# Optimization experiments

Measured on AMD Instinct MI355X. Metric: run time of the kernel, lower is better.

## Reference

```python
import jax, jax.numpy as jnp
import numpy as np

N, E, D, H = 100000, 1250000, 64, 128
EPS = 1e-5


def sage_bn_relu(x, src, dst, W_self, b_self, W_neigh, gamma, beta):
    # mean aggregation over in-neighbors (DGL SAGEConv 'mean')
    n = x.shape[0]
    deg = jax.ops.segment_sum(jnp.ones((src.shape[0],), x.dtype), dst, num_segments=n)
    agg = jax.ops.segment_sum(x[src], dst, num_segments=n)  # [N, d]
    neigh = agg / jnp.maximum(deg, 1.0)[:, None]             # zero in-degree -> 0
    h = x @ W_self + b_self + neigh @ W_neigh                # fc_self + fc_neigh
    # BatchNorm1d (training-mode batch statistics, biased variance)
    mu = h.mean(0)
    var = jnp.mean((h - mu) ** 2, axis=0)
    h = (h - mu) * jax.lax.rsqrt(var + EPS) * gamma + beta
    return jax.nn.relu(h)  # dropout omitted (deterministic eval)


def setup_inputs() -> dict:
    key = jax.random.key(0)
    ks = jax.random.split(key, 32)
    inp = {
        "x": jax.random.normal(ks[0], (N, D), jnp.float32),
        "src": jax.random.randint(ks[1], (E,), 0, N),
        "dst": jax.random.randint(ks[2], (E,), 0, N),
    }
    dims = [(D, H), (H, H), (H, H)]
    k = 3
    for i, (din, dout) in enumerate(dims):
        s = 1.0 / np.sqrt(din)
        inp[f"W_self{i}"] = jax.random.uniform(ks[k], (din, dout), jnp.float32, -s, s); k += 1
        inp[f"b_self{i}"] = jnp.zeros((dout,), jnp.float32)
        inp[f"W_neigh{i}"] = jax.random.uniform(ks[k], (din, dout), jnp.float32, -s, s); k += 1
        inp[f"gamma{i}"] = jnp.ones((dout,), jnp.float32)
        inp[f"beta{i}"] = jnp.zeros((dout,), jnp.float32)
    s = 1.0 / np.sqrt(H)
    inp["Wc"] = jax.random.uniform(ks[k], (H, 2), jnp.float32, -s, s)
    inp["bc"] = jnp.zeros((2,), jnp.float32)
    return inp


def reference(x, src, dst,
              W_self0, b_self0, W_neigh0, gamma0, beta0,
              W_self1, b_self1, W_neigh1, gamma1, beta1,
              W_self2, b_self2, W_neigh2, gamma2, beta2,
              Wc, bc):
    h = sage_bn_relu(x, src, dst, W_self0, b_self0, W_neigh0, gamma0, beta0)
    h = sage_bn_relu(h, src, dst, W_self1, b_self1, W_neigh1, gamma1, beta1)
    h = sage_bn_relu(h, src, dst, W_self2, b_self2, W_neigh2, gamma2, beta2)
    return h @ Wc + bc  # [N, 2]
```

## Files before the change

### kernel.cpp

```cpp
#include <hip/hip_runtime.h>


#define N_NODES 100000
#define N_EDGES 1250000
#define NB 1042
#define BSZ 96
#define CAP 1536
#define BPART 256
#define INVN (1.0f / 100000.0f)

typedef short bf16x8 __attribute__((ext_vector_type(8)));
typedef float f32x4 __attribute__((ext_vector_type(4)));
typedef unsigned short u16x8 __attribute__((ext_vector_type(8)));
typedef unsigned short u16x4 __attribute__((ext_vector_type(4)));

__device__ __forceinline__ float bf2f(unsigned short u) {
  union { unsigned int i; float f; } c; c.i = ((unsigned int)u) << 16; return c.f;
}
__device__ __forceinline__ unsigned short f2bf(float f) {
  union { float f; unsigned int i; } c; c.f = f;
  unsigned int r = (c.i + 0x7FFFu + ((c.i >> 16) & 1u)) >> 16;
  return (unsigned short)r;
}
__device__ __forceinline__ void bn_st(const float* stats, const float* gam,
                                      const float* bet, int c, float& s, float& t) {
  float sum = stats[c] + stats[256 + c] + stats[512 + c] + stats[768 + c];
  float sq  = stats[128 + c] + stats[384 + c] + stats[640 + c] + stats[896 + c];
  float mu = sum * INVN;
  float var = sq * INVN - mu * mu;
  s = gam[c] * rsqrtf(var + 1e-5f);
  t = bet[c] - mu * s;
}
__device__ __forceinline__ void gload_lds16(const void* g, void* l) {
  __builtin_amdgcn_global_load_lds(
      (const __attribute__((address_space(1))) unsigned int*)g,
      (__attribute__((address_space(3))) unsigned int*)l, 16, 0, 0);
}

__global__ __launch_bounds__(256) void k_prep(
    const float* __restrict__ x, unsigned short* __restrict__ x16,
    const float* __restrict__ W0s, const float* __restrict__ W0n,
    const float* __restrict__ W1s, const float* __restrict__ W1n,
    const float* __restrict__ W2s, const float* __restrict__ W2n,
    unsigned short* __restrict__ wt, int* __restrict__ gcursor,
    float* __restrict__ stats3) {
  int blk = blockIdx.x, t = threadIdx.x;
  if (blk < 6250) {
    int i = blk * 256 + t;
    float4 v = ((const float4*)x)[i];
    u16x4 o;
    o.x = f2bf(v.x); o.y = f2bf(v.y); o.z = f2bf(v.z); o.w = f2bf(v.w);
    ((u16x4*)x16)[i] = o;
  } else if (blk < 6570) {
    int i = (blk - 6250) * 256 + t;
    if (i < 16384) {
      const float* W = (i < 8192) ? W0s : W0n;
      unsigned short* o = wt + (i < 8192 ? 0 : 8192);
      int j = i & 8191;
      int c = j >> 6, k = j & 63;
      o[j] = f2bf(W[k * 128 + c]);
    } else {
      int j = i - 16384;
      int sel = j >> 14;
      j &= 16383;
      const float* W = (sel == 0) ? W1s : (sel == 1) ? W1n : (sel == 2) ? W2s : W2n;
      unsigned short* o = wt + 16384 + sel * 16384;
      int c = j >> 7, k = j & 127;
      o[j] = f2bf(W[k * 128 + c]);
    }
  } else {
    for (int i = t; i < NB; i += 256) gcursor[i] = 0;
    for (int i = t; i < 3 * 1024; i += 256) stats3[i] = 0.f;
  }
}

__global__ __launch_bounds__(256) void k_hist(const int* __restrict__ dst,
                                              int* __restrict__ hist, int E) {
  __shared__ int h[NB];
  int t = threadIdx.x;
  int chunk = (E + BPART - 1) / BPART;
  int start = blockIdx.x * chunk;
  int end = min(E, start + chunk);
  for (int b = t; b < NB; b += 256) h[b] = 0;
  __syncthreads();
  for (int e = start + t; e < end; e += 256) atomicAdd(&h[dst[e] / BSZ], 1);
  __syncthreads();
  for (int b = t; b < NB; b += 256) hist[blockIdx.x * NB + b] = h[b];
}

__global__ __launch_bounds__(256) void k_scan(const int* __restrict__ hist,
                                              int* __restrict__ base,
                                              int* __restrict__ gcursor) {
  int bb = blockIdx.x * 256 + threadIdx.x;
  if (bb >= NB) return;
  int run = 0;
  for (int r0 = 0; r0 < BPART; r0 += 16) {
    int v[16];
    #pragma unroll
    for (int u = 0; u < 16; u++) v[u] = hist[(r0 + u) * NB + bb];
    #pragma unroll
    for (int u = 0; u < 16; u++) { base[(r0 + u) * NB + bb] = run; run += v[u]; }
  }
  gcursor[bb] = run;
}

__global__ __launch_bounds__(256) void k_scatter(const int* __restrict__ src,
                                                 const int* __restrict__ dst,
                                                 const int* __restrict__ base,
                                                 unsigned int* __restrict__ part, int E) {
  __shared__ int cur[NB];
  int t = threadIdx.x;
  int chunk = (E + BPART - 1) / BPART;
  int start = blockIdx.x * chunk;
  int end = min(E, start + chunk);
  for (int b = t; b < NB; b += 256) cur[b] = base[blockIdx.x * NB + b];
  __syncthreads();
  for (int e = start + t; e < end; e += 256) {
    int d = dst[e];
    int b = d / BSZ;
    int pos = atomicAdd(&cur[b], 1);
    if ((unsigned)pos < (unsigned)CAP)
      part[(size_t)b * CAP + pos] = (unsigned)src[e] | ((unsigned)(d - b * BSZ) << 17);
  }
}

template <int DIM>
__global__ __launch_bounds__(512) void k_aggb(const unsigned short* __restrict__ h,
                                              const unsigned int* __restrict__ part,
                                              const int* __restrict__ gcursor,
                                              unsigned short* __restrict__ neigh, int n,
                                              const float* __restrict__ statsP,
                                              const float* __restrict__ gamP,
                                              const float* __restrict__ betP) {
  __shared__ unsigned eraw[CAP];
  __shared__ unsigned eord[CAP];
  __shared__ int cnt[BSZ], offv[BSZ], cur[BSZ];
  __shared__ int scan[128];
  int t = threadIdx.x;
  int bkt = blockIdx.x;
  int node0 = bkt * BSZ;
  int nn = min(BSZ, n - node0);
  if (nn <= 0) return;
  if (t < BSZ) cnt[t] = 0;
  __syncthreads();
  int ec = gcursor[bkt];
  ec = max(0, min(ec, CAP));
  for (int i = t; i < ec; i += 512) {
    unsigned w = part[(size_t)bkt * CAP + i];
    eraw[i] = w;
    atomicAdd(&cnt[w >> 17], 1);
  }
  __syncthreads();
  if (t < 128) scan[t] = (t < BSZ) ? cnt[t] : 0;
  __syncthreads();
  #pragma unroll
  for (int o = 1; o < 128; o <<= 1) {
    int x = 0;
    if (t < 128 && t >= o) x = scan[t - o];
    __syncthreads();
    if (t < 128) scan[t] += x;
    __syncthreads();
  }
  if (t < BSZ) { offv[t] = scan[t] - cnt[t]; cur[t] = scan[t] - cnt[t]; }
  __syncthreads();
  for (int i = t; i < ec; i += 512) {
    unsigned w = eraw[i];
    int p = atomicAdd(&cur[w >> 17], 1);
    eord[p] = w & 0x1FFFF;
  }
  __syncthreads();
  const int G = DIM / 8, NG = 512 / G;
  int gid = t / G, li = t % G;
  float sreg[8], treg[8];
  bool bn = (statsP != nullptr);
  if (bn) {
    #pragma unroll
    for (int k = 0; k < 8; k++) bn_st(statsP, gamP, betP, li * 8 + k, sreg[k], treg[k]);
  }
  for (int nd = gid; nd < nn; nd += NG) {
    int s = offv[nd], c = cnt[nd];
    int e = s + c;
    float acc[8] = {0.f, 0.f, 0.f, 0.f, 0.f, 0.f, 0.f, 0.f};
    int j = s;
    for (; j + 4 <= e; j += 4) {
      int sn0 = eord[j], sn1 = eord[j + 1], sn2 = eord[j + 2], sn3 = eord[j + 3];
      u16x8 v0 = *(const u16x8*)&h[(size_t)sn0 * DIM + li * 8];
      u16x8 v1 = *(const u16x8*)&h[(size_t)sn1 * DIM + li * 8];
      u16x8 v2 = *(const u16x8*)&h[(size_t)sn2 * DIM + li * 8];
      u16x8 v3 = *(const u16x8*)&h[(size_t)sn3 * DIM + li * 8];
      if (bn) {
        #pragma unroll
        for (int k = 0; k < 8; k++)
          acc[k] += fmaxf(fmaf(bf2f(v0[k]), sreg[k], treg[k]), 0.f)
                  + fmaxf(fmaf(bf2f(v1[k]), sreg[k], treg[k]), 0.f)
                  + fmaxf(fmaf(bf2f(v2[k]), sreg[k], treg[k]), 0.f)
                  + fmaxf(fmaf(bf2f(v3[k]), sreg[k], treg[k]), 0.f);
      } else {
        #pragma unroll
        for (int k = 0; k < 8; k++)
          acc[k] += (bf2f(v0[k]) + bf2f(v1[k])) + (bf2f(v2[k]) + bf2f(v3[k]));
      }
    }
    for (; j + 2 <= e; j += 2) {
      int sn0 = eord[j], sn1 = eord[j + 1];
      u16x8 v0 = *(const u16x8*)&h[(size_t)sn0 * DIM + li * 8];
      u16x8 v1 = *(const u16x8*)&h[(size_t)sn1 * DIM + li * 8];
      if (bn) {
        #pragma unroll
        for (int k = 0; k < 8; k++)
          acc[k] += fmaxf(fmaf(bf2f(v0[k]), sreg[k], treg[k]), 0.f)
                  + fmaxf(fmaf(bf2f(v1[k]), sreg[k], treg[k]), 0.f);
      } else {
        #pragma unroll
        for (int k = 0; k < 8; k++) acc[k] += bf2f(v0[k]) + bf2f(v1[k]);
      }
    }
    if (j < e) {
      int sn = eord[j];
      u16x8 v = *(const u16x8*)&h[(size_t)sn * DIM + li * 8];
      if (bn) {
        #pragma unroll
        for (int k = 0; k < 8; k++)
          acc[k] += fmaxf(fmaf(bf2f(v[k]), sreg[k], treg[k]), 0.f);
      } else {
        #pragma unroll
        for (int k = 0; k < 8; k++) acc[k] += bf2f(v[k]);
      }
    }
    float inv = 1.0f / fmaxf((float)c, 1.0f);
    u16x8 o;
    #pragma unroll
    for (int k = 0; k < 8; k++) o[k] = f2bf(acc[k] * inv);
    *(u16x8*)&neigh[(size_t)(node0 + nd) * DIM + li * 8] = o;
  }
}

__global__ __launch_bounds__(256) void k_gemm_mfma(
    const unsigned short* __restrict__ A1, const unsigned short* __restrict__ W1t,
    const unsigned short* __restrict__ A2, const unsigned short* __restrict__ W2t,
    const float* __restrict__ bias, unsigned short* __restrict__ C,
    float* __restrict__ stats, int M, int din,
    const float* __restrict__ statsP, const float* __restrict__ gamP,
    const float* __restrict__ betP) {
  __shared__ unsigned short As[2][128 * 32];
  __shared__ unsigned short Bs[2][128 * 32];
  __shared__ float redS[4 * 128];
  __shared__ float redQ[4 * 128];
  __shared__ float sBN[128], tBN[128];

  int t = threadIdx.x;
  int lane = t & 63, w = t >> 6;
  int l15 = lane & 15, quad = lane >> 4;
  int row0 = blockIdx.x * 128;
  bool hasBN = (statsP != nullptr);
  if (hasBN && t < 128) bn_st(statsP, gamP, betP, t, sBN[t], tBN[t]);
  if (hasBN) __syncthreads();

  const int steps1 = din >> 5;
  const int S = steps1 * 2;

  f32x4 acc[2][8];
  #pragma unroll
  for (int rt = 0; rt < 2; rt++)
    #pragma unroll
    for (int ct = 0; ct < 8; ct++) acc[rt][ct] = (f32x4){0.f, 0.f, 0.f, 0.f};

  auto Aof  = [&](int s) { return (s < steps1) ? A1 : A2; };
  auto Wof  = [&](int s) { return (s < steps1) ? W1t : W2t; };
  auto k0of = [&](int s) { return ((s < steps1) ? s : s - steps1) << 5; };

  auto stageA_async = [&](int s, int bi) {
    const unsigned short* A = Aof(s); int k0 = k0of(s);
    #pragma unroll
    for (int i = 0; i < 2; i++) {
      int idx = t + 256 * i;
      int r = idx >> 2, prt = idx & 3;
      gload_lds16(&A[(size_t)(row0 + r) * din + k0 + prt * 8],
                  &As[bi][(i * 256 + w * 64) * 8]);
    }
  };
  auto stageB = [&](int s, int bi) {
    const unsigned short* Wt = Wof(s); int k0 = k0of(s);
    #pragma unroll
    for (int i = 0; i < 2; i++) {
      int idx = t + 256 * i;
      int r = idx >> 2, prt = idx & 3;
      gload_lds16(&Wt[(size_t)r * din + k0 + prt * 8],
                  &Bs[bi][(i * 256 + w * 64) * 8]);
    }
  };
  u16x8 vreg[2];
  auto bnLoad = [&](int s) {
    const unsigned short* A = Aof(s); int k0 = k0of(s);
    #pragma unroll
    for (int i = 0; i < 2; i++) {
      int idx = t + 256 * i;
      int r = idx >> 2, prt = idx & 3;
      int row = row0 + r;
      vreg[i] = (u16x8){0, 0, 0, 0, 0, 0, 0, 0};
      if (row < M) vreg[i] = *(const u16x8*)&A[(size_t)row * din + k0 + prt * 8];
    }
  };
  auto bnWrite = [&](int s, int bi) {
    int k0 = k0of(s);
    #pragma unroll
    for (int i = 0; i < 2; i++) {
      int idx = t + 256 * i;
      int prt = idx & 3;
      u16x8 v = vreg[i];
      #pragma unroll
      for (int j = 0; j < 8; j++) {
        int c = k0 + prt * 8 + j;
        v[j] = f2bf(fmaxf(fmaf(bf2f(v[j]), sBN[c], tBN[c]), 0.f));
      }
      *(u16x8*)&As[bi][idx * 8] = v;
    }
  };

  if (hasBN) { bnLoad(0); stageB(0, 0); bnWrite(0, 0); }
  else       { stageA_async(0, 0); stageB(0, 0); }
  __syncthreads();

  int cb = 0;
  for (int s = 0; s < S; s++) {
    int nb = cb ^ 1;
    bool haveNext = (s + 1 < S);
    bool bnNext = hasBN && (s + 1 < steps1);
    if (haveNext) {
      if (bnNext) bnLoad(s + 1);
      else        stageA_async(s + 1, nb);
      stageB(s + 1, nb);
    }
    bf16x8 af[2], bfr[8];
    #pragma unroll
    for (int rt = 0; rt < 2; rt++)
      af[rt] = *(const bf16x8*)&As[cb][(w * 32 + rt * 16 + l15) * 32 + quad * 8];
    #pragma unroll
    for (int ct = 0; ct < 8; ct++)
      bfr[ct] = *(const bf16x8*)&Bs[cb][(ct * 16 + l15) * 32 + quad * 8];
    #pragma unroll
    for (int rt = 0; rt < 2; rt++)
      #pragma unroll
      for (int ct = 0; ct < 8; ct++)
        acc[rt][ct] = __builtin_amdgcn_mfma_f32_16x16x32_bf16(af[rt], bfr[ct], acc[rt][ct], 0, 0, 0);
    if (haveNext) {
      if (bnNext) bnWrite(s + 1, nb);
      __syncthreads();
    }
    cb = nb;
  }

  float bcol[8], ls[8], lq[8];
  #pragma unroll
  for (int ct = 0; ct < 8; ct++) {
    bcol[ct] = bias[ct * 16 + l15];
    ls[ct] = 0.f; lq[ct] = 0.f;
  }
  #pragma unroll
  for (int rt = 0; rt < 2; rt++) {
    #pragma unroll
    for (int r = 0; r < 4; r++) {
      int row = row0 + w * 32 + rt * 16 + quad * 4 + r;
      if (row < M) {
        #pragma unroll
        for (int ct = 0; ct < 8; ct++) {
          float v = acc[rt][ct][r] + bcol[ct];
          C[(size_t)row * 128 + ct * 16 + l15] = f2bf(v);
          ls[ct] += v; lq[ct] += v * v;
        }
      }
    }
  }
  #pragma unroll
  for (int ct = 0; ct < 8; ct++) {
    ls[ct] += __shfl_xor(ls[ct], 16); ls[ct] += __shfl_xor(ls[ct], 32);
    lq[ct] += __shfl_xor(lq[ct], 16); lq[ct] += __shfl_xor(lq[ct], 32);
  }
  if (quad == 0) {
    #pragma unroll
    for (int ct = 0; ct < 8; ct++) {
      redS[w * 128 + ct * 16 + l15] = ls[ct];
      redQ[w * 128 + ct * 16 + l15] = lq[ct];
    }
  }
  __syncthreads();
  if (t < 128) {
    float s = redS[t] + redS[128 + t] + redS[256 + t] + redS[384 + t];
    float q = redQ[t] + redQ[128 + t] + redQ[256 + t] + redQ[384 + t];
    int rep = (blockIdx.x & 3) * 256;
    atomicAdd(&stats[rep + t], s);
    atomicAdd(&stats[rep + 128 + t], q);
  }
}

__global__ void k_final(const unsigned short* __restrict__ h,
                        const float* __restrict__ statsP, const float* __restrict__ gamP,
                        const float* __restrict__ betP, const float* __restrict__ Wc,
                        const float* __restrict__ bc, float* __restrict__ out, int n) {
  int lane = threadIdx.x & 63;
  int row = blockIdx.x * (blockDim.x >> 6) + (threadIdx.x >> 6);
  if (row >= n) return;
  float acc0 = 0.f, acc1 = 0.f;
  #pragma unroll
  for (int m = 0; m < 2; m++) {
    int c = lane + 64 * m;
    float s, tt;
    bn_st(statsP, gamP, betP, c, s, tt);
    float v = bf2f(h[(size_t)row * 128 + c]);
    v = fmaxf(fmaf(v, s, tt), 0.f);
    acc0 += v * Wc[c * 2 + 0];
    acc1 += v * Wc[c * 2 + 1];
  }
  #pragma unroll
  for (int off = 32; off > 0; off >>= 1) {
    acc0 += __shfl_down(acc0, off);
    acc1 += __shfl_down(acc1, off);
  }
  if (lane == 0) {
    out[row * 2 + 0] = acc0 + bc[0];
    out[row * 2 + 1] = acc1 + bc[1];
  }
}

extern "C" void kernel_launch(void* const* d_in, const int* in_sizes, int n_in,
                              void* d_out, int out_size, void* d_ws, size_t ws_size,
                              hipStream_t stream) {
  const float* x   = (const float*)d_in[0];
  const int* src   = (const int*)d_in[1];
  const int* dst   = (const int*)d_in[2];
  const float* Wself[3] = {(const float*)d_in[3], (const float*)d_in[8],  (const float*)d_in[13]};
  const float* bself[3] = {(const float*)d_in[4], (const float*)d_in[9],  (const float*)d_in[14]};
  const float* Wngh[3]  = {(const float*)d_in[5], (const float*)d_in[10], (const float*)d_in[15]};
  const float* gam[3]   = {(const float*)d_in[6], (const float*)d_in[11], (const float*)d_in[16]};
  const float* bet[3]   = {(const float*)d_in[7], (const float*)d_in[12], (const float*)d_in[17]};
  const float* Wc = (const float*)d_in[18];
  const float* bc = (const float*)d_in[19];
  float* out = (float*)d_out;

  const int N = N_NODES, E = N_EDGES;

  unsigned short* x16 = (unsigned short*)d_ws;
  unsigned short* b0  = x16 + (size_t)N * 64;
  unsigned short* b1  = b0 + (size_t)N * 128;
  unsigned short* b2  = b1 + (size_t)N * 128;
  unsigned short* wt  = b2 + (size_t)N * 128;
  unsigned int* part  = (unsigned int*)(wt + 81920);
  int* gcursor  = (int*)(part + (size_t)NB * CAP);
  float* stats3 = (float*)(gcursor + NB);

  int* hist = (int*)b1;
  int* base = hist + (size_t)BPART * NB;

  k_prep<<<6571, 256, 0, stream>>>(x, x16, Wself[0], Wngh[0], Wself[1], Wngh[1],
                                   Wself[2], Wngh[2], wt, gcursor, stats3);

  k_hist<<<BPART, 256, 0, stream>>>(dst, hist, E);
  k_scan<<<(NB + 255) / 256, 256, 0, stream>>>(hist, base, gcursor);
  k_scatter<<<BPART, 256, 0, stream>>>(src, dst, base, part, E);

  const int gemmBlocks = (N + 127) / 128;

  k_aggb<64><<<NB, 512, 0, stream>>>(x16, part, gcursor, b0, N, nullptr, nullptr, nullptr);
  k_gemm_mfma<<<gemmBlocks, 256, 0, stream>>>(x16, wt + 0, b0, wt + 8192, bself[0],
                                              b1, stats3 + 0, N, 64,
                                              nullptr, nullptr, nullptr);

  k_aggb<128><<<NB, 512, 0, stream>>>(b1, part, gcursor, b0, N,
                                      stats3 + 0, gam[0], bet[0]);
  k_gemm_mfma<<<gemmBlocks, 256, 0, stream>>>(b1, wt + 16384, b0, wt + 32768, bself[1],
                                              b2, stats3 + 1024, N, 128,
                                              stats3 + 0, gam[0], bet[0]);

  k_aggb<128><<<NB, 512, 0, stream>>>(b2, part, gcursor, b0, N,
                                      stats3 + 1024, gam[1], bet[1]);
  k_gemm_mfma<<<gemmBlocks, 256, 0, stream>>>(b2, wt + 49152, b0, wt + 65536, bself[2],
                                              b1, stats3 + 2048, N, 128,
                                              stats3 + 1024, gam[1], bet[1]);

  k_final<<<(N + 3) / 4, 256, 0, stream>>>(b1, stats3 + 2048, gam[2], bet[2],
                                           Wc, bc, out, N);
}
```

Measured before the change: 398.9 us.

## Unfuse BatchNorm+ReLU into a standalone in-place pass before aggregation

```diff
diff --git a/kernel.cpp b/kernel.cpp
--- a/kernel.cpp
+++ b/kernel.cpp
@@ -42,8 +42,7 @@
     const float* __restrict__ W0s, const float* __restrict__ W0n,
     const float* __restrict__ W1s, const float* __restrict__ W1n,
     const float* __restrict__ W2s, const float* __restrict__ W2n,
-    unsigned short* __restrict__ wt, int* __restrict__ gcursor,
-    float* __restrict__ stats3) {
+    unsigned short* __restrict__ wt, float* __restrict__ stats3) {
   int blk = blockIdx.x, t = threadIdx.x;
   if (blk < 6250) {
     int i = blk * 256 + t;
@@ -69,7 +68,6 @@
       o[j] = f2bf(W[k * 128 + c]);
     }
   } else {
-    for (int i = t; i < NB; i += 256) gcursor[i] = 0;
     for (int i = t; i < 3 * 1024; i += 256) stats3[i] = 0.f;
   }
 }
@@ -124,14 +122,29 @@
   }
 }
 
+__global__ __launch_bounds__(256) void k_bnrelu(unsigned short* __restrict__ h,
+                                                const float* __restrict__ statsP,
+                                                const float* __restrict__ gamP,
+                                                const float* __restrict__ betP, int n8) {
+  __shared__ float sS[128], sT[128];
+  int t = threadIdx.x;
+  if (t < 128) bn_st(statsP, gamP, betP, t, sS[t], sT[t]);
+  __syncthreads();
+  int i = blockIdx.x * 256 + t;
+  if (i >= n8) return;
+  int c0 = (i & 15) * 8;
+  u16x8 v = ((const u16x8*)h)[i];
+  #pragma unroll
+  for (int j = 0; j < 8; j++)
+    v[j] = f2bf(fmaxf(fmaf(bf2f(v[j]), sS[c0 + j], sT[c0 + j]), 0.f));
+  ((u16x8*)h)[i] = v;
+}
+
 template <int DIM>
 __global__ __launch_bounds__(512) void k_aggb(const unsigned short* __restrict__ h,
                                               const unsigned int* __restrict__ part,
                                               const int* __restrict__ gcursor,
-                                              unsigned short* __restrict__ neigh, int n,
-                                              const float* __restrict__ statsP,
-                                              const float* __restrict__ gamP,
-                                              const float* __restrict__ betP) {
+                                              unsigned short* __restrict__ neigh, int n) {
   __shared__ unsigned eraw[CAP];
   __shared__ unsigned eord[CAP];
   __shared__ int cnt[BSZ], offv[BSZ], cur[BSZ];
@@ -171,61 +184,23 @@
   __syncthreads();
   const int G = DIM / 8, NG = 512 / G;
   int gid = t / G, li = t % G;
-  float sreg[8], treg[8];
-  bool bn = (statsP != nullptr);
-  if (bn) {
-    #pragma unroll
-    for (int k = 0; k < 8; k++) bn_st(statsP, gamP, betP, li * 8 + k, sreg[k], treg[k]);
-  }
   for (int nd = gid; nd < nn; nd += NG) {
     int s = offv[nd], c = cnt[nd];
     int e = s + c;
     float acc[8] = {0.f, 0.f, 0.f, 0.f, 0.f, 0.f, 0.f, 0.f};
     int j = s;
-    for (; j + 4 <= e; j += 4) {
-      int sn0 = eord[j], sn1 = eord[j + 1], sn2 = eord[j + 2], sn3 = eord[j + 3];
-      u16x8 v0 = *(const u16x8*)&h[(size_t)sn0 * DIM + li * 8];
-      u16x8 v1 = *(const u16x8*)&h[(size_t)sn1 * DIM + li * 8];
-      u16x8 v2 = *(const u16x8*)&h[(size_t)sn2 * DIM + li * 8];
-      u16x8 v3 = *(const u16x8*)&h[(size_t)sn3 * DIM + li * 8];
-      if (bn) {
-        #pragma unroll
-        for (int k = 0; k < 8; k++)
-          acc[k] += fmaxf(fmaf(bf2f(v0[k]), sreg[k], treg[k]), 0.f)
-                  + fmaxf(fmaf(bf2f(v1[k]), sreg[k], treg[k]), 0.f)
-                  + fmaxf(fmaf(bf2f(v2[k]), sreg[k], treg[k]), 0.f)
-                  + fmaxf(fmaf(bf2f(v3[k]), sreg[k], treg[k]), 0.f);
-      } else {
-        #pragma unroll
-        for (int k = 0; k < 8; k++)
-          acc[k] += (bf2f(v0[k]) + bf2f(v1[k])) + (bf2f(v2[k]) + bf2f(v3[k]));
-      }
-    }
     for (; j + 2 <= e; j += 2) {
       int sn0 = eord[j], sn1 = eord[j + 1];
       u16x8 v0 = *(const u16x8*)&h[(size_t)sn0 * DIM + li * 8];
       u16x8 v1 = *(const u16x8*)&h[(size_t)sn1 * DIM + li * 8];
-      if (bn) {
-        #pragma unroll
-        for (int k = 0; k < 8; k++)
-          acc[k] += fmaxf(fmaf(bf2f(v0[k]), sreg[k], treg[k]), 0.f)
-                  + fmaxf(fmaf(bf2f(v1[k]), sreg[k], treg[k]), 0.f);
-      } else {
-        #pragma unroll
-        for (int k = 0; k < 8; k++) acc[k] += bf2f(v0[k]) + bf2f(v1[k]);
-      }
+      #pragma unroll
+      for (int k = 0; k < 8; k++) acc[k] += bf2f(v0[k]) + bf2f(v1[k]);
     }
     if (j < e) {
       int sn = eord[j];
       u16x8 v = *(const u16x8*)&h[(size_t)sn * DIM + li * 8];
-      if (bn) {
-        #pragma unroll
-        for (int k = 0; k < 8; k++)
-          acc[k] += fmaxf(fmaf(bf2f(v[k]), sreg[k], treg[k]), 0.f);
-      } else {
-        #pragma unroll
-        for (int k = 0; k < 8; k++) acc[k] += bf2f(v[k]);
-      }
+      #pragma unroll
+      for (int k = 0; k < 8; k++) acc[k] += bf2f(v[k]);
     }
     float inv = 1.0f / fmaxf((float)c, 1.0f);
     u16x8 o;
@@ -239,22 +214,16 @@
     const unsigned short* __restrict__ A1, const unsigned short* __restrict__ W1t,
     const unsigned short* __restrict__ A2, const unsigned short* __restrict__ W2t,
     const float* __restrict__ bias, unsigned short* __restrict__ C,
-    float* __restrict__ stats, int M, int din,
-    const float* __restrict__ statsP, const float* __restrict__ gamP,
-    const float* __restrict__ betP) {
+    float* __restrict__ stats, int M, int din) {
   __shared__ unsigned short As[2][128 * 32];
   __shared__ unsigned short Bs[2][128 * 32];
   __shared__ float redS[4 * 128];
   __shared__ float redQ[4 * 128];
-  __shared__ float sBN[128], tBN[128];
 
   int t = threadIdx.x;
   int lane = t & 63, w = t >> 6;
   int l15 = lane & 15, quad = lane >> 4;
   int row0 = blockIdx.x * 128;
-  bool hasBN = (statsP != nullptr);
-  if (hasBN && t < 128) bn_st(statsP, gamP, betP, t, sBN[t], tBN[t]);
-  if (hasBN) __syncthreads();
 
   const int steps1 = din >> 5;
   const int S = steps1 * 2;
@@ -269,7 +238,7 @@
   auto Wof  = [&](int s) { return (s < steps1) ? W1t : W2t; };
   auto k0of = [&](int s) { return ((s < steps1) ? s : s - steps1) << 5; };
 
-  auto stageA_async = [&](int s, int bi) {
+  auto stageA = [&](int s, int bi) {
     const unsigned short* A = Aof(s); int k0 = k0of(s);
     #pragma unroll
     for (int i = 0; i < 2; i++) {
@@ -289,48 +258,15 @@
                   &Bs[bi][(i * 256 + w * 64) * 8]);
     }
   };
-  u16x8 vreg[2];
-  auto bnLoad = [&](int s) {
-    const unsigned short* A = Aof(s); int k0 = k0of(s);
-    #pragma unroll
-    for (int i = 0; i < 2; i++) {
-      int idx = t + 256 * i;
-      int r = idx >> 2, prt = idx & 3;
-      int row = row0 + r;
-      vreg[i] = (u16x8){0, 0, 0, 0, 0, 0, 0, 0};
-      if (row < M) vreg[i] = *(const u16x8*)&A[(size_t)row * din + k0 + prt * 8];
-    }
-  };
-  auto bnWrite = [&](int s, int bi) {
-    int k0 = k0of(s);
-    #pragma unroll
-    for (int i = 0; i < 2; i++) {
-      int idx = t + 256 * i;
-      int prt = idx & 3;
-      u16x8 v = vreg[i];
-      #pragma unroll
-      for (int j = 0; j < 8; j++) {
-        int c = k0 + prt * 8 + j;
-        v[j] = f2bf(fmaxf(fmaf(bf2f(v[j]), sBN[c], tBN[c]), 0.f));
-      }
-      *(u16x8*)&As[bi][idx * 8] = v;
-    }
-  };
-
-  if (hasBN) { bnLoad(0); stageB(0, 0); bnWrite(0, 0); }
-  else       { stageA_async(0, 0); stageB(0, 0); }
+
+  stageA(0, 0); stageB(0, 0);
   __syncthreads();
 
   int cb = 0;
   for (int s = 0; s < S; s++) {
     int nb = cb ^ 1;
     bool haveNext = (s + 1 < S);
-    bool bnNext = hasBN && (s + 1 < steps1);
-    if (haveNext) {
-      if (bnNext) bnLoad(s + 1);
-      else        stageA_async(s + 1, nb);
-      stageB(s + 1, nb);
-    }
+    if (haveNext) { stageA(s + 1, nb); stageB(s + 1, nb); }
     bf16x8 af[2], bfr[8];
     #pragma unroll
     for (int rt = 0; rt < 2; rt++)
@@ -343,10 +279,7 @@
       #pragma unroll
       for (int ct = 0; ct < 8; ct++)
         acc[rt][ct] = __builtin_amdgcn_mfma_f32_16x16x32_bf16(af[rt], bfr[ct], acc[rt][ct], 0, 0, 0);
-    if (haveNext) {
-      if (bnNext) bnWrite(s + 1, nb);
-      __syncthreads();
-    }
+    if (haveNext) __syncthreads();
     cb = nb;
   }
 
@@ -452,30 +385,28 @@
   int* base = hist + (size_t)BPART * NB;
 
   k_prep<<<6571, 256, 0, stream>>>(x, x16, Wself[0], Wngh[0], Wself[1], Wngh[1],
-                                   Wself[2], Wngh[2], wt, gcursor, stats3);
+                                   Wself[2], Wngh[2], wt, stats3);
 
   k_hist<<<BPART, 256, 0, stream>>>(dst, hist, E);
   k_scan<<<(NB + 255) / 256, 256, 0, stream>>>(hist, base, gcursor);
   k_scatter<<<BPART, 256, 0, stream>>>(src, dst, base, part, E);
 
   const int gemmBlocks = (N + 127) / 128;
-
-  k_aggb<64><<<NB, 512, 0, stream>>>(x16, part, gcursor, b0, N, nullptr, nullptr, nullptr);
+  const int bnBlocks = (N * 16 + 255) / 256;
+
+  k_aggb<64><<<NB, 512, 0, stream>>>(x16, part, gcursor, b0, N);
   k_gemm_mfma<<<gemmBlocks, 256, 0, stream>>>(x16, wt + 0, b0, wt + 8192, bself[0],
-                                              b1, stats3 + 0, N, 64,
-                                              nullptr, nullptr, nullptr);
-
-  k_aggb<128><<<NB, 512, 0, stream>>>(b1, part, gcursor, b0, N,
-                                      stats3 + 0, gam[0], bet[0]);
+                                              b1, stats3 + 0, N, 64);
+  k_bnrelu<<<bnBlocks, 256, 0, stream>>>(b1, stats3 + 0, gam[0], bet[0], N * 16);
+
+  k_aggb<128><<<NB, 512, 0, stream>>>(b1, part, gcursor, b0, N);
   k_gemm_mfma<<<gemmBlocks, 256, 0, stream>>>(b1, wt + 16384, b0, wt + 32768, bself[1],
-                                              b2, stats3 + 1024, N, 128,
-                                              stats3 + 0, gam[0], bet[0]);
-
-  k_aggb<128><<<NB, 512, 0, stream>>>(b2, part, gcursor, b0, N,
-                                      stats3 + 1024, gam[1], bet[1]);
+                                              b2, stats3 + 1024, N, 128);
+  k_bnrelu<<<bnBlocks, 256, 0, stream>>>(b2, stats3 + 1024, gam[1], bet[1], N * 16);
+
+  k_aggb<128><<<NB, 512, 0, stream>>>(b2, part, gcursor, b0, N);
   k_gemm_mfma<<<gemmBlocks, 256, 0, stream>>>(b2, wt + 49152, b0, wt + 65536, bself[2],
-                                              b1, stats3 + 2048, N, 128,
-                                              stats3 + 1024, gam[1], bet[1]);
+                                              b1, stats3 + 2048, N, 128);
 
   k_final<<<(N + 3) / 4, 256, 0, stream>>>(b1, stats3 + 2048, gam[2], bet[2],
                                            Wc, bc, out, N);
```

After: 416.5 us. 4.4% more time.

## Fuse neighbor aggregation into per-layer MFMA GEMM kernel via LDS tile

Applied to the files above, without the earlier changes.

```diff
diff --git a/kernel.cpp b/kernel.cpp
--- a/kernel.cpp
+++ b/kernel.cpp
@@ -3,9 +3,9 @@
 
 #define N_NODES 100000
 #define N_EDGES 1250000
-#define NB 1042
-#define BSZ 96
-#define CAP 1536
+#define NB 782
+#define BSZ 128
+#define CAP 2048
 #define BPART 256
 #define INVN (1.0f / 100000.0f)
 
@@ -36,14 +36,19 @@
       (const __attribute__((address_space(1))) unsigned int*)g,
       (__attribute__((address_space(3))) unsigned int*)l, 16, 0, 0);
 }
+template <int DIN>
+__device__ __forceinline__ int nswz(int row, int c) {
+  return row * DIN + (c ^ ((row & (DIN == 128 ? 15 : 7)) << 3));
+}
 
 __global__ __launch_bounds__(256) void k_prep(
     const float* __restrict__ x, unsigned short* __restrict__ x16,
     const float* __restrict__ W0s, const float* __restrict__ W0n,
     const float* __restrict__ W1s, const float* __restrict__ W1n,
     const float* __restrict__ W2s, const float* __restrict__ W2n,
-    unsigned short* __restrict__ wt, int* __restrict__ gcursor,
-    float* __restrict__ stats3) {
+    unsigned short* __restrict__ wt, float* __restrict__ stats3,
+    const int* __restrict__ dst, int* __restrict__ hist, int E) {
+  __shared__ int hh[NB];
   int blk = blockIdx.x, t = threadIdx.x;
   if (blk < 6250) {
     int i = blk * 256 + t;
@@ -68,24 +73,19 @@
       int c = j >> 7, k = j & 127;
       o[j] = f2bf(W[k * 128 + c]);
     }
+  } else if (blk == 6570) {
+    for (int i = t; i < 3 * 1024; i += 256) stats3[i] = 0.f;
   } else {
-    for (int i = t; i < NB; i += 256) gcursor[i] = 0;
-    for (int i = t; i < 3 * 1024; i += 256) stats3[i] = 0.f;
-  }
-}
-
-__global__ __launch_bounds__(256) void k_hist(const int* __restrict__ dst,
-                                              int* __restrict__ hist, int E) {
-  __shared__ int h[NB];
-  int t = threadIdx.x;
-  int chunk = (E + BPART - 1) / BPART;
-  int start = blockIdx.x * chunk;
-  int end = min(E, start + chunk);
-  for (int b = t; b < NB; b += 256) h[b] = 0;
-  __syncthreads();
-  for (int e = start + t; e < end; e += 256) atomicAdd(&h[dst[e] / BSZ], 1);
-  __syncthreads();
-  for (int b = t; b < NB; b += 256) hist[blockIdx.x * NB + b] = h[b];
+    int hb = blk - 6571;
+    int chunk = (E + BPART - 1) / BPART;
+    int start = hb * chunk;
+    int end = min(E, start + chunk);
+    for (int b = t; b < NB; b += 256) hh[b] = 0;
+    __syncthreads();
+    for (int e = start + t; e < end; e += 256) atomicAdd(&hh[dst[e] >> 7], 1);
+    __syncthreads();
+    for (int b = t; b < NB; b += 256) hist[hb * NB + b] = hh[b];
+  }
 }
 
 __global__ __launch_bounds__(256) void k_scan(const int* __restrict__ hist,
@@ -117,224 +117,205 @@
   __syncthreads();
   for (int e = start + t; e < end; e += 256) {
     int d = dst[e];
-    int b = d / BSZ;
+    int b = d >> 7;
     int pos = atomicAdd(&cur[b], 1);
     if ((unsigned)pos < (unsigned)CAP)
-      part[(size_t)b * CAP + pos] = (unsigned)src[e] | ((unsigned)(d - b * BSZ) << 17);
-  }
-}
-
-template <int DIM>
-__global__ __launch_bounds__(512) void k_aggb(const unsigned short* __restrict__ h,
-                                              const unsigned int* __restrict__ part,
-                                              const int* __restrict__ gcursor,
-                                              unsigned short* __restrict__ neigh, int n,
-                                              const float* __restrict__ statsP,
-                                              const float* __restrict__ gamP,
-                                              const float* __restrict__ betP) {
-  __shared__ unsigned eraw[CAP];
-  __shared__ unsigned eord[CAP];
-  __shared__ int cnt[BSZ], offv[BSZ], cur[BSZ];
-  __shared__ int scan[128];
-  int t = threadIdx.x;
-  int bkt = blockIdx.x;
-  int node0 = bkt * BSZ;
-  int nn = min(BSZ, n - node0);
-  if (nn <= 0) return;
-  if (t < BSZ) cnt[t] = 0;
-  __syncthreads();
-  int ec = gcursor[bkt];
-  ec = max(0, min(ec, CAP));
-  for (int i = t; i < ec; i += 512) {
-    unsigned w = part[(size_t)bkt * CAP + i];
-    eraw[i] = w;
-    atomicAdd(&cnt[w >> 17], 1);
-  }
-  __syncthreads();
-  if (t < 128) scan[t] = (t < BSZ) ? cnt[t] : 0;
-  __syncthreads();
-  #pragma unroll
-  for (int o = 1; o < 128; o <<= 1) {
-    int x = 0;
-    if (t < 128 && t >= o) x = scan[t - o];
-    __syncthreads();
-    if (t < 128) scan[t] += x;
-    __syncthreads();
-  }
-  if (t < BSZ) { offv[t] = scan[t] - cnt[t]; cur[t] = scan[t] - cnt[t]; }
-  __syncthreads();
-  for (int i = t; i < ec; i += 512) {
-    unsigned w = eraw[i];
-    int p = atomicAdd(&cur[w >> 17], 1);
-    eord[p] = w & 0x1FFFF;
-  }
-  __syncthreads();
-  const int G = DIM / 8, NG = 512 / G;
-  int gid = t / G, li = t % G;
-  float sreg[8], treg[8];
-  bool bn = (statsP != nullptr);
-  if (bn) {
-    #pragma unroll
-    for (int k = 0; k < 8; k++) bn_st(statsP, gamP, betP, li * 8 + k, sreg[k], treg[k]);
-  }
-  for (int nd = gid; nd < nn; nd += NG) {
-    int s = offv[nd], c = cnt[nd];
-    int e = s + c;
-    float acc[8] = {0.f, 0.f, 0.f, 0.f, 0.f, 0.f, 0.f, 0.f};
-    int j = s;
-    for (; j + 4 <= e; j += 4) {
-      int sn0 = eord[j], sn1 = eord[j + 1], sn2 = eord[j + 2], sn3 = eord[j + 3];
-      u16x8 v0 = *(const u16x8*)&h[(size_t)sn0 * DIM + li * 8];
-      u16x8 v1 = *(const u16x8*)&h[(size_t)sn1 * DIM + li * 8];
-      u16x8 v2 = *(const u16x8*)&h[(size_t)sn2 * DIM + li * 8];
-      u16x8 v3 = *(const u16x8*)&h[(size_t)sn3 * DIM + li * 8];
-      if (bn) {
-        #pragma unroll
-        for (int k = 0; k < 8; k++)
-          acc[k] += fmaxf(fmaf(bf2f(v0[k]), sreg[k], treg[k]), 0.f)
-                  + fmaxf(fmaf(bf2f(v1[k]), sreg[k], treg[k]), 0.f)
-                  + fmaxf(fmaf(bf2f(v2[k]), sreg[k], treg[k]), 0.f)
-                  + fmaxf(fmaf(bf2f(v3[k]), sreg[k], treg[k]), 0.f);
-      } else {
-        #pragma unroll
-        for (int k = 0; k < 8; k++)
-          acc[k] += (bf2f(v0[k]) + bf2f(v1[k])) + (bf2f(v2[k]) + bf2f(v3[k]));
-      }
-    }
-    for (; j + 2 <= e; j += 2) {
-      int sn0 = eord[j], sn1 = eord[j + 1];
-      u16x8 v0 = *(const u16x8*)&h[(size_t)sn0 * DIM + li * 8];
-      u16x8 v1 = *(const u16x8*)&h[(size_t)sn1 * DIM + li * 8];
-      if (bn) {
-        #pragma unroll
-        for (int k = 0; k < 8; k++)
-          acc[k] += fmaxf(fmaf(bf2f(v0[k]), sreg[k], treg[k]), 0.f)
-                  + fmaxf(fmaf(bf2f(v1[k]), sreg[k], treg[k]), 0.f);
-      } else {
-        #pragma unroll
-        for (int k = 0; k < 8; k++) acc[k] += bf2f(v0[k]) + bf2f(v1[k]);
-      }
-    }
-    if (j < e) {
-      int sn = eord[j];
-      u16x8 v = *(const u16x8*)&h[(size_t)sn * DIM + li * 8];
-      if (bn) {
-        #pragma unroll
-        for (int k = 0; k < 8; k++)
-          acc[k] += fmaxf(fmaf(bf2f(v[k]), sreg[k], treg[k]), 0.f);
-      } else {
-        #pragma unroll
-        for (int k = 0; k < 8; k++) acc[k] += bf2f(v[k]);
-      }
-    }
-    float inv = 1.0f / fmaxf((float)c, 1.0f);
-    u16x8 o;
-    #pragma unroll
-    for (int k = 0; k < 8; k++) o[k] = f2bf(acc[k] * inv);
-    *(u16x8*)&neigh[(size_t)(node0 + nd) * DIM + li * 8] = o;
-  }
-}
-
-__global__ __launch_bounds__(256) void k_gemm_mfma(
-    const unsigned short* __restrict__ A1, const unsigned short* __restrict__ W1t,
-    const unsigned short* __restrict__ A2, const unsigned short* __restrict__ W2t,
-    const float* __restrict__ bias, unsigned short* __restrict__ C,
-    float* __restrict__ stats, int M, int din,
+      part[(size_t)b * CAP + pos] = (unsigned)src[e] | ((unsigned)(d & 127) << 17);
+  }
+}
+
+template <int DIN, bool BN>
+__global__ __launch_bounds__(256) void k_layer(
+    const unsigned short* __restrict__ h, const unsigned short* __restrict__ W1t,
+    const unsigned short* __restrict__ W2t, const float* __restrict__ bias,
+    const unsigned int* __restrict__ part, const int* __restrict__ gcursor,
+    unsigned short* __restrict__ C, float* __restrict__ stats, int M,
     const float* __restrict__ statsP, const float* __restrict__ gamP,
     const float* __restrict__ betP) {
   __shared__ unsigned short As[2][128 * 32];
   __shared__ unsigned short Bs[2][128 * 32];
-  __shared__ float redS[4 * 128];
-  __shared__ float redQ[4 * 128];
+  __shared__ unsigned short neighT[128 * DIN];
+  __shared__ unsigned eord[CAP];
+  __shared__ int cnt[BSZ], offv[BSZ], cur[BSZ];
   __shared__ float sBN[128], tBN[128];
+  unsigned* eraw = (unsigned*)&As[0][0];
+  float* redS = (float*)&eord[0];
+  float* redQ = redS + 512;
 
   int t = threadIdx.x;
   int lane = t & 63, w = t >> 6;
   int l15 = lane & 15, quad = lane >> 4;
-  int row0 = blockIdx.x * 128;
-  bool hasBN = (statsP != nullptr);
-  if (hasBN && t < 128) bn_st(statsP, gamP, betP, t, sBN[t], tBN[t]);
-  if (hasBN) __syncthreads();
-
-  const int steps1 = din >> 5;
+  int bkt = blockIdx.x;
+  int node0 = bkt * BSZ;
+  int row0 = node0;
+  int nn = min(BSZ, M - node0);
+
+  if (t < BSZ) cnt[t] = 0;
+  if (BN && t < 128) bn_st(statsP, gamP, betP, t, sBN[t], tBN[t]);
+  __syncthreads();
+  int ec = gcursor[bkt];
+  ec = max(0, min(ec, CAP));
+  for (int i = t; i < ec; i += 256) {
+    unsigned wd = part[(size_t)bkt * CAP + i];
+    eraw[i] = wd;
+    atomicAdd(&cnt[wd >> 17], 1);
+  }
+  __syncthreads();
+  if (t < BSZ) offv[t] = cnt[t];
+  __syncthreads();
+  #pragma unroll
+  for (int o = 1; o < BSZ; o <<= 1) {
+    int xv = 0;
+    if (t < BSZ && t >= o) xv = offv[t - o];
+    __syncthreads();
+    if (t < BSZ) offv[t] += xv;
+    __syncthreads();
+  }
+  if (t < BSZ) { int ex = offv[t] - cnt[t]; offv[t] = ex; cur[t] = ex; }
+  __syncthreads();
+  for (int i = t; i < ec; i += 256) {
+    unsigned wd = eraw[i];
+    int p = atomicAdd(&cur[wd >> 17], 1);
+    eord[p] = wd & 0x1FFFF;
+  }
+  __syncthreads();
+
+  const int G = DIN / 8, NG = 256 / G;
+  int gid = t / G, li = t % G;
+  float sreg[8], treg[8];
+  if (BN) {
+    #pragma unroll
+    for (int k = 0; k < 8; k++) { sreg[k] = sBN[li * 8 + k]; treg[k] = tBN[li * 8 + k]; }
+  }
+  for (int nd = gid; nd < BSZ; nd += NG) {
+    u16x8 o;
+    if (nd >= nn) {
+      #pragma unroll
+      for (int k = 0; k < 8; k++) o[k] = 0;
+    } else {
+      int s0 = offv[nd], c = cnt[nd];
+      int e = s0 + c;
+      float acc[8] = {0.f, 0.f, 0.f, 0.f, 0.f, 0.f, 0.f, 0.f};
+      int j = s0;
+      for (; j + 4 <= e; j += 4) {
+        int a0 = eord[j], a1 = eord[j + 1], a2 = eord[j + 2], a3 = eord[j + 3];
+        u16x8 v0 = *(const u16x8*)&h[(size_t)a0 * DIN + li * 8];
+        u16x8 v1 = *(const u16x8*)&h[(size_t)a1 * DIN + li * 8];
+        u16x8 v2 = *(const u16x8*)&h[(size_t)a2 * DIN + li * 8];
+        u16x8 v3 = *(const u16x8*)&h[(size_t)a3 * DIN + li * 8];
+        if (BN) {
+          #pragma unroll
+          for (int k = 0; k < 8; k++)
+            acc[k] += fmaxf(fmaf(bf2f(v0[k]), sreg[k], treg[k]), 0.f)
+                    + fmaxf(fmaf(bf2f(v1[k]), sreg[k], treg[k]), 0.f)
+                    + fmaxf(fmaf(bf2f(v2[k]), sreg[k], treg[k]), 0.f)
+                    + fmaxf(fmaf(bf2f(v3[k]), sreg[k], treg[k]), 0.f);
+        } else {
+          #pragma unroll
+          for (int k = 0; k < 8; k++)
+            acc[k] += (bf2f(v0[k]) + bf2f(v1[k])) + (bf2f(v2[k]) + bf2f(v3[k]));
+        }
+      }
+      for (; j < e; j++) {
+        int a0 = eord[j];
+        u16x8 v0 = *(const u16x8*)&h[(size_t)a0 * DIN + li * 8];
+        #pragma unroll
+        for (int k = 0; k < 8; k++) {
+          float f = bf2f(v0[k]);
+          acc[k] += BN ? fmaxf(fmaf(f, sreg[k], treg[k]), 0.f) : f;
+        }
+      }
+      float inv = 1.0f / fmaxf((float)c, 1.0f);
+      #pragma unroll
+      for (int k = 0; k < 8; k++) o[k] = f2bf(acc[k] * inv);
+    }
+    *(u16x8*)&neighT[nswz<DIN>(nd, li * 8)] = o;
+  }
+  __syncthreads();
+
+  const int steps1 = DIN / 32;
   const int S = steps1 * 2;
-
   f32x4 acc[2][8];
   #pragma unroll
   for (int rt = 0; rt < 2; rt++)
     #pragma unroll
     for (int ct = 0; ct < 8; ct++) acc[rt][ct] = (f32x4){0.f, 0.f, 0.f, 0.f};
 
-  auto Aof  = [&](int s) { return (s < steps1) ? A1 : A2; };
-  auto Wof  = [&](int s) { return (s < steps1) ? W1t : W2t; };
-  auto k0of = [&](int s) { return ((s < steps1) ? s : s - steps1) << 5; };
-
-  auto stageA_async = [&](int s, int bi) {
-    const unsigned short* A = Aof(s); int k0 = k0of(s);
+  auto stageA = [&](int s, int bi) {
+    int k0 = s * 32;
     #pragma unroll
     for (int i = 0; i < 2; i++) {
       int idx = t + 256 * i;
       int r = idx >> 2, prt = idx & 3;
-      gload_lds16(&A[(size_t)(row0 + r) * din + k0 + prt * 8],
+      gload_lds16(&h[(size_t)(row0 + r) * DIN + k0 + prt * 8],
                   &As[bi][(i * 256 + w * 64) * 8]);
     }
   };
   auto stageB = [&](int s, int bi) {
-    const unsigned short* Wt = Wof(s); int k0 = k0of(s);
+    const unsigned short* Wt = (s < steps1) ? W1t : W2t;
+    int k0 = (s < steps1 ? s : s - steps1) * 32;
     #pragma unroll
     for (int i = 0; i < 2; i++) {
       int idx = t + 256 * i;
       int r = idx >> 2, prt = idx & 3;
-      gload_lds16(&Wt[(size_t)r * din + k0 + prt * 8],
+      gload_lds16(&Wt[(size_t)r * DIN + k0 + prt * 8],
                   &Bs[bi][(i * 256 + w * 64) * 8]);
     }
   };
   u16x8 vreg[2];
   auto bnLoad = [&](int s) {
-    const unsigned short* A = Aof(s); int k0 = k0of(s);
+    int k0 = s * 32;
     #pragma unroll
     for (int i = 0; i < 2; i++) {
       int idx = t + 256 * i;
       int r = idx >> 2, prt = idx & 3;
       int row = row0 + r;
       vreg[i] = (u16x8){0, 0, 0, 0, 0, 0, 0, 0};
-      if (row < M) vreg[i] = *(const u16x8*)&A[(size_t)row * din + k0 + prt * 8];
+      if (row < M) vreg[i] = *(const u16x8*)&h[(size_t)row * DIN + k0 + prt * 8];
     }
   };
   auto bnWrite = [&](int s, int bi) {
-    int k0 = k0of(s);
+    int k0 = s * 32;
     #pragma unroll
     for (int i = 0; i < 2; i++) {
       int idx = t + 256 * i;
       int prt = idx & 3;
       u16x8 v = vreg[i];
       #pragma unroll
-      for (int j = 0; j < 8; j++) {
-        int c = k0 + prt * 8 + j;
-        v[j] = f2bf(fmaxf(fmaf(bf2f(v[j]), sBN[c], tBN[c]), 0.f));
+      for (int j2 = 0; j2 < 8; j2++) {
+        int c = k0 + prt * 8 + j2;
+        v[j2] = f2bf(fmaxf(fmaf(bf2f(v[j2]), sBN[c], tBN[c]), 0.f));
       }
       *(u16x8*)&As[bi][idx * 8] = v;
     }
   };
 
-  if (hasBN) { bnLoad(0); stageB(0, 0); bnWrite(0, 0); }
-  else       { stageA_async(0, 0); stageB(0, 0); }
+  if (BN) { bnLoad(0); stageB(0, 0); bnWrite(0, 0); }
+  else    { stageA(0, 0); stageB(0, 0); }
   __syncthreads();
 
   int cb = 0;
   for (int s = 0; s < S; s++) {
     int nb = cb ^ 1;
     bool haveNext = (s + 1 < S);
-    bool bnNext = hasBN && (s + 1 < steps1);
+    bool nextA1 = (s + 1 < steps1);
     if (haveNext) {
-      if (bnNext) bnLoad(s + 1);
-      else        stageA_async(s + 1, nb);
+      if (nextA1) { if (BN) bnLoad(s + 1); else stageA(s + 1, nb); }
       stageB(s + 1, nb);
     }
     bf16x8 af[2], bfr[8];
-    #pragma unroll
-    for (int rt = 0; rt < 2; rt++)
-      af[rt] = *(const bf16x8*)&As[cb][(w * 32 + rt * 16 + l15) * 32 + quad * 8];
+    if (s < steps1) {
+      #pragma unroll
+      for (int rt = 0; rt < 2; rt++)
+        af[rt] = *(const bf16x8*)&As[cb][(w * 32 + rt * 16 + l15) * 32 + quad * 8];
+    } else {
+      int c0 = (s - steps1) * 32 + quad * 8;
+      #pragma unroll
+      for (int rt = 0; rt < 2; rt++) {
+        int row = w * 32 + rt * 16 + l15;
+        af[rt] = *(const bf16x8*)&neighT[nswz<DIN>(row, c0)];
+      }
+    }
     #pragma unroll
     for (int ct = 0; ct < 8; ct++)
       bfr[ct] = *(const bf16x8*)&Bs[cb][(ct * 16 + l15) * 32 + quad * 8];
@@ -344,7 +325,7 @@
       for (int ct = 0; ct < 8; ct++)
         acc[rt][ct] = __builtin_amdgcn_mfma_f32_16x16x32_bf16(af[rt], bfr[ct], acc[rt][ct], 0, 0, 0);
     if (haveNext) {
-      if (bnNext) bnWrite(s + 1, nb);
+      if (nextA1 && BN) bnWrite(s + 1, nb);
       __syncthreads();
     }
     cb = nb;
@@ -440,8 +421,7 @@
   const int N = N_NODES, E = N_EDGES;
 
   unsigned short* x16 = (unsigned short*)d_ws;
-  unsigned short* b0  = x16 + (size_t)N * 64;
-  unsigned short* b1  = b0 + (size_t)N * 128;
+  unsigned short* b1  = x16 + (size_t)N * 64;
   unsigned short* b2  = b1 + (size_t)N * 128;
   unsigned short* wt  = b2 + (size_t)N * 128;
   unsigned int* part  = (unsigned int*)(wt + 81920);
@@ -451,31 +431,22 @@
   int* hist = (int*)b1;
   int* base = hist + (size_t)BPART * NB;
 
-  k_prep<<<6571, 256, 0, stream>>>(x, x16, Wself[0], Wngh[0], Wself[1], Wngh[1],
-                                   Wself[2], Wngh[2], wt, gcursor, stats3);
-
-  k_hist<<<BPART, 256, 0, stream>>>(dst, hist, E);
+  k_prep<<<6571 + BPART, 256, 0, stream>>>(x, x16, Wself[0], Wngh[0], Wself[1],
+                                           Wngh[1], Wself[2], Wngh[2], wt, stats3,
+                                           dst, hist, E);
+
   k_scan<<<(NB + 255) / 256, 256, 0, stream>>>(hist, base, gcursor);
   k_scatter<<<BPART, 256, 0, stream>>>(src, dst, base, part, E);
 
-  const int gemmBlocks = (N + 127) / 128;
-
-  k_aggb<64><<<NB, 512, 0, stream>>>(x16, part, gcursor, b0, N, nullptr, nullptr, nullptr);
-  k_gemm_mfma<<<gemmBlocks, 256, 0, stream>>>(x16, wt + 0, b0, wt + 8192, bself[0],
-                                              b1, stats3 + 0, N, 64,
-                                              nullptr, nullptr, nullptr);
-
-  k_aggb<128><<<NB, 512, 0, stream>>>(b1, part, gcursor, b0, N,
-                                      stats3 + 0, gam[0], bet[0]);
-  k_gemm_mfma<<<gemmBlocks, 256, 0, stream>>>(b1, wt + 16384, b0, wt + 32768, bself[1],
-                                              b2, stats3 + 1024, N, 128,
-                                              stats3 + 0, gam[0], bet[0]);
-
-  k_aggb<128><<<NB, 512, 0, stream>>>(b2, part, gcursor, b0, N,
-                                      stats3 + 1024, gam[1], bet[1]);
-  k_gemm_mfma<<<gemmBlocks, 256, 0, stream>>>(b2, wt + 49152, b0, wt + 65536, bself[2],
-                                              b1, stats3 + 2048, N, 128,
-                                              stats3 + 1024, gam[1], bet[1]);
+  k_layer<64, false><<<NB, 256, 0, stream>>>(
+      x16, wt + 0, wt + 8192, bself[0], part, gcursor, b1, stats3 + 0, N,
+      nullptr, nullptr, nullptr);
+  k_layer<128, true><<<NB, 256, 0, stream>>>(
+      b1, wt + 16384, wt + 32768, bself[1], part, gcursor, b2, stats3 + 1024, N,
+      stats3 + 0, gam[0], bet[0]);
+  k_layer<128, true><<<NB, 256, 0, stream>>>(
+      b2, wt + 49152, wt + 65536, bself[2], part, gcursor, b1, stats3 + 2048, N,
+      stats3 + 1024, gam[1], bet[1]);
 
   k_final<<<(N + 3) / 4, 256, 0, stream>>>(b1, stats3 + 2048, gam[2], bet[2],
                                            Wc, bc, out, N);
```

Measured after the change: 411.6 us. +3.2%, slower.
